# Kernel tuning notes

Hardware: AMD Instinct MI355X
Metric: run time of the kernel (lower is better)

The kernel has to match this reference:

```python
import jax, jax.numpy as jnp
import numpy as np

# Config (mirrors init_kwargs)
N_PARTS = 4
N_DATASETS = 4
N_VOLUMES = 12
N_TRANSFORMS = 1
TEMP = 0.1
EPS = 1e-6
BS = N_PARTS * N_DATASETS * N_VOLUMES          # 192
N = BS * (N_TRANSFORMS + 1)                    # 384 total rows
PD = N_PARTS * N_DATASETS                      # 16
C, H, W = 32, 48, 48


def setup_inputs() -> dict:
    key = jax.random.key(0)
    k1, k2 = jax.random.split(key)
    reg_pred = jax.random.normal(k1, (N, C, H, W), dtype=jnp.float32)
    mean_representations = jax.random.normal(k2, (N_DATASETS, C, H, W), dtype=jnp.float32)
    return {"reg_pred": reg_pred, "mean_representations": mean_representations}


def reference(reg_pred, mean_representations):
    X = reg_pred.reshape(N, -1)                                  # [N, D]
    ds_id = (jnp.arange(N) // N_PARTS) % N_DATASETS              # dataset id per row
    Mn = mean_representations.reshape(N_DATASETS, -1)[ds_id]     # [N, D] per-row mean
    Z = X - Mn                                                   # demeaned
    # cosine similarity with per-vector norm clamped at eps (torch CosineSimilarity)
    nrm = jnp.maximum(jnp.linalg.norm(Z, axis=1), EPS)
    Zn = Z / nrm[:, None]
    S = (Zn @ Zn.T) / TEMP                                       # [N, N] scaled cos sims
    E = jnp.exp(S)
    # negative (denominator) set for anchor a: all j with j % PD != a % PD
    rem = jnp.arange(N) % PD
    neg_mask = rem[:, None] != rem[None, :]
    Dsum = jnp.sum(E * neg_mask, axis=1)                         # [N]

    p = jnp.arange(BS)
    i1 = p
    i2 = BS + p
    i3 = (p + PD) % N
    i4 = (BS + p + PD) % N

    def pair_loss(a, b):
        # Faithful to original: BOTH terms use the (a,b) numerator similarity
        num = S[a, b]
        en = jnp.exp(num)
        return -(num - jnp.log(en + Dsum[a])) - (num - jnp.log(en + Dsum[b]))

    total = (pair_loss(i1, i2) + pair_loss(i3, i4)
             + pair_loss(i1, i3) + pair_loss(i2, i4)).sum()
    return total / (N_TRANSFORMS * 3 * BS)
```

## Files before the change

kernel.cpp:

```cpp
#include <hip/hip_runtime.h>
#include <hip/hip_bf16.h>
#include <stdint.h>

#define NR 384
#define DD 73728
#define PDV 16
#define KSPLIT 128
#define KCH 576
#define BK 32
#define NIT 18
#define RS 40
#define TILE_F 16384
#define KSTRIDE (9 * TILE_F)

typedef __bf16 bf16;
typedef __attribute__((ext_vector_type(4))) __bf16 bf16x4;
typedef __attribute__((ext_vector_type(8))) __bf16 bf16x8;
typedef __attribute__((ext_vector_type(4))) float f32x4;

__global__ __launch_bounds__(256, 3) void k_gram(const float* __restrict__ X,
                                                 const float* __restrict__ M,
                                                 float* __restrict__ Gp9,
                                                 float* __restrict__ Dp,
                                                 unsigned* __restrict__ ctr) {
    __shared__ float msh[4 * KCH];
    __shared__ __align__(16) char sbuf[41984];
    bf16* ash = (bf16*)sbuf;
    bf16* bsh = (bf16*)(sbuf + 20480);

    const int tid  = threadIdx.x;
    const int lane = tid & 63;
    const int w    = tid >> 6;
    const int quad = lane >> 4;
    const int l15  = lane & 15;
    const int wm   = w & 1, wn = w >> 1;
    const int srow = tid >> 3;
    const int fseg = tid & 7;
    const int mds  = (srow >> 2) & 3;

    if (blockIdx.x == 0 && tid == 0) *ctr = 0u;

    int xcd  = blockIdx.x & 7;
    int g    = blockIdx.x >> 3;
    int tile = g % 6;
    int ks   = xcd + 8 * (g / 6);
    int tm = (tile < 3) ? 0 : ((tile < 5) ? 1 : 2);
    int tn = (tile < 3) ? tile : ((tile < 5) ? (tile - 2) : 2);
    const bool diag = (tm == tn);
    const float* Xa = X + (size_t)(tm * 128) * DD;
    const float* Xb = X + (size_t)(tn * 128) * DD;
    size_t k0 = (size_t)ks * KCH;

    for (int i = tid; i < 4 * 144; i += 256) {
        int ds = i / 144;
        int c  = (i - ds * 144) * 4;
        *(float4*)&msh[ds * KCH + c] = *(const float4*)(M + (size_t)ds * DD + k0 + c);
    }

    f32x4 acc[4][4];
#pragma unroll
    for (int i = 0; i < 4; ++i)
#pragma unroll
        for (int j = 0; j < 4; ++j) acc[i][j] = (f32x4){0.f, 0.f, 0.f, 0.f};

    float4 xa[4], xb[4];
    auto load_regs = [&](int it) {
        size_t gk = k0 + (size_t)it * BK + fseg * 4;
#pragma unroll
        for (int p = 0; p < 4; ++p) {
            int row = p * 32 + srow;
            xa[p] = *(const float4*)(Xa + (size_t)row * DD + gk);
            if (!diag) xb[p] = *(const float4*)(Xb + (size_t)row * DD + gk);
        }
    };
    auto write_tiles = [&](int it, int buf) {
        int kc = it * BK + fseg * 4;
        float4 m4 = *(const float4*)&msh[mds * KCH + kc];
#pragma unroll
        for (int p = 0; p < 4; ++p) {
            int row = p * 32 + srow;
            bf16x4 za;
            za[0] = (bf16)(xa[p].x - m4.x); za[1] = (bf16)(xa[p].y - m4.y);
            za[2] = (bf16)(xa[p].z - m4.z); za[3] = (bf16)(xa[p].w - m4.w);
            *(bf16x4*)&ash[buf * 5120 + row * RS + fseg * 4] = za;
            if (!diag) {
                bf16x4 zb;
                zb[0] = (bf16)(xb[p].x - m4.x); zb[1] = (bf16)(xb[p].y - m4.y);
                zb[2] = (bf16)(xb[p].z - m4.z); zb[3] = (bf16)(xb[p].w - m4.w);
                *(bf16x4*)&bsh[buf * 5120 + row * RS + fseg * 4] = zb;
            }
        }
    };
    auto compute = [&](int buf) {
        const bf16* bb = diag ? (ash + buf * 5120) : (bsh + buf * 5120);
        bf16x8 af[4], bfv[4];
#pragma unroll
        for (int i = 0; i < 4; ++i) {
            int r = wm * 64 + i * 16 + l15;
            af[i] = *(const bf16x8*)&ash[buf * 5120 + r * RS + quad * 8];
        }
#pragma unroll
        for (int j = 0; j < 4; ++j) {
            int r = wn * 64 + j * 16 + l15;
            bfv[j] = *(const bf16x8*)&bb[r * RS + quad * 8];
        }
#pragma unroll
        for (int i = 0; i < 4; ++i)
#pragma unroll
            for (int j = 0; j < 4; ++j)
                acc[i][j] = __builtin_amdgcn_mfma_f32_16x16x32_bf16(
                    af[i], bfv[j], acc[i][j], 0, 0, 0);
    };

    load_regs(0);
    __syncthreads();
    write_tiles(0, 0);
    load_regs(1);
    __syncthreads();

    for (int it = 0; it < NIT; ++it) {
        int buf = it & 1;
        if (it + 1 < NIT) {
            write_tiles(it + 1, buf ^ 1);
            if (it + 2 < NIT) load_regs(it + 2);
        }
        compute(buf);
        __syncthreads();
    }

    float* gp = Gp9 + (size_t)ks * KSTRIDE + (size_t)(tm * 3 + tn) * TILE_F;
#pragma unroll
    for (int i = 0; i < 4; ++i) {
        int lr0 = wm * 64 + i * 16 + quad * 4;
#pragma unroll
        for (int j = 0; j < 4; ++j) {
            int lc = wn * 64 + j * 16 + l15;
#pragma unroll
            for (int r = 0; r < 4; ++r)
                gp[(lr0 + r) * 128 + lc] = acc[i][j][r];
        }
    }

    if (diag) {
        if (wm == wn && (l15 >> 2) == quad) {
#pragma unroll
            for (int i = 0; i < 4; ++i)
                Dp[(size_t)ks * NR + tm * 128 + wm * 64 + i * 16 + l15] =
                    acc[i][i][l15 & 3];
        }
    } else {
        float* tb = (float*)sbuf;
        float* gpT = Gp9 + (size_t)ks * KSTRIDE + (size_t)(tn * 3 + tm) * TILE_F;
#pragma unroll
        for (int h = 0; h < 2; ++h) {
            __syncthreads();
            if (wm == h) {
#pragma unroll
                for (int i = 0; i < 4; ++i) {
                    int rr0 = i * 16 + quad * 4;
#pragma unroll
                    for (int j = 0; j < 4; ++j) {
                        int cc = wn * 64 + j * 16 + l15;
#pragma unroll
                        for (int r = 0; r < 4; ++r)
                            tb[(rr0 + r) * 129 + cc] = acc[i][j][r];
                    }
                }
            }
            __syncthreads();
#pragma unroll
            for (int rep = 0; rep < 32; ++rep) {
                int idx = rep * 256 + tid;
                int c = idx >> 6;
                int r = idx & 63;
                gpT[c * 128 + h * 64 + r] = tb[r * 129 + c];
            }
        }
    }
}

__global__ __launch_bounds__(384) void k_tail(const float* __restrict__ Gp9,
                                              const float* __restrict__ Dp,
                                              float* __restrict__ rt,
                                              unsigned* __restrict__ ctr,
                                              float* __restrict__ out) {
    __shared__ float invn_sh[NR];
    __shared__ float sv[NR];
    __shared__ float wred[6];
    __shared__ bool amlast;

    const int tid  = threadIdx.x;
    const int lane = tid & 63;
    const int w    = tid >> 6;
    const int b    = tid;
    const int a    = blockIdx.x;

    float s2 = 0.f;
    const float* dp = Dp + b;
#pragma unroll 8
    for (int ks = 0; ks < KSPLIT; ++ks) s2 += dp[(size_t)ks * NR];
    invn_sh[b] = 1.f / fmaxf(sqrtf(s2), 1e-6f);
    __syncthreads();

    const int pa = a >> 7, pb = b >> 7;
    const float* gbase = Gp9 + (size_t)(pa * 3 + pb) * TILE_F
                       + (size_t)(a & 127) * 128 + (b & 127);
    float gsum = 0.f;
#pragma unroll 8
    for (int ks = 0; ks < KSPLIT; ++ks) gsum += gbase[(size_t)ks * KSTRIDE];

    const float ia = invn_sh[a];
    const float s  = gsum * ia * invn_sh[b] * 10.0f;
    sv[b] = s;
    float e = ((b & 15) != (a & 15)) ? expf(s) : 0.f;
#pragma unroll
    for (int o = 32; o > 0; o >>= 1) e += __shfl_down(e, o);
    if (lane == 0) wred[w] = e;
    __syncthreads();

    if (tid == 0) {
        float Dsa = wred[0] + wred[1] + wred[2] + wred[3] + wred[4] + wred[5];
        int pr[4];
        if (a < 16)       { pr[0] = 192 + a; pr[1] = a + 16;  pr[2] = a + 192; pr[3] = a + 368; }
        else if (a < 192) { pr[0] = 192 + a; pr[1] = a + 16;  pr[2] = a + 192; pr[3] = a - 16; }
        else if (a < 368) { pr[0] = a - 192; pr[1] = a + 16;  pr[2] = a - 192; pr[3] = a - 16; }
        else              { pr[0] = a - 192; pr[1] = a - 368; pr[2] = a - 192; pr[3] = a - 16; }
        float t = 0.f;
#pragma unroll
        for (int sidx = 0; sidx < 4; ++sidx) {
            float num = sv[pr[sidx]];
            t += -num + logf(expf(num) + Dsa);
        }
        rt[a] = t;
        __threadfence();
        amlast = (atomicAdd(ctr, 1u) == (unsigned)(NR - 1));
    }
    __syncthreads();

    if (amlast) {
        __threadfence();
        float v = rt[tid];
#pragma unroll
        for (int o = 32; o > 0; o >>= 1) v += __shfl_down(v, o);
        if (lane == 0) wred[w] = v;
        __syncthreads();
        if (tid == 0)
            out[0] = (wred[0] + wred[1] + wred[2] + wred[3] + wred[4] + wred[5])
                     * (1.0f / 576.0f);
    }
}

extern "C" void kernel_launch(void* const* d_in, const int* in_sizes, int n_in,
                              void* d_out, int out_size, void* d_ws, size_t ws_size,
                              hipStream_t stream) {
    const float* X = (const float*)d_in[0];
    const float* M = (const float*)d_in[1];
    float* out = (float*)d_out;

    char* ws = (char*)d_ws;
    float* Gp9 = (float*)ws;
    float* Dp  = Gp9 + (size_t)KSPLIT * KSTRIDE;
    float* rt  = Dp + (size_t)KSPLIT * NR;
    unsigned* ctr = (unsigned*)(rt + NR);

    k_gram<<<dim3(6 * KSPLIT), dim3(256), 0, stream>>>(X, M, Gp9, Dp, ctr);
    k_tail<<<dim3(NR), dim3(384), 0, stream>>>(Gp9, Dp, rt, ctr, out);
}
```

Measured before the change: 205.1 us.

## Fuse gram and tail kernels with a grid-wide atomic barrier

```diff
diff --git a/kernel.cpp b/kernel.cpp
--- a/kernel.cpp
+++ b/kernel.cpp
@@ -4,7 +4,6 @@
 
 #define NR 384
 #define DD 73728
-#define PDV 16
 #define KSPLIT 128
 #define KCH 576
 #define BK 32
@@ -12,18 +11,26 @@
 #define RS 40
 #define TILE_F 16384
 #define KSTRIDE (9 * TILE_F)
+#define NBLK (6 * KSPLIT)
 
 typedef __bf16 bf16;
 typedef __attribute__((ext_vector_type(4))) __bf16 bf16x4;
 typedef __attribute__((ext_vector_type(8))) __bf16 bf16x8;
 typedef __attribute__((ext_vector_type(4))) float f32x4;
 
-__global__ __launch_bounds__(256, 3) void k_gram(const float* __restrict__ X,
-                                                 const float* __restrict__ M,
-                                                 float* __restrict__ Gp9,
-                                                 float* __restrict__ Dp,
-                                                 unsigned* __restrict__ ctr) {
-    __shared__ float msh[4 * KCH];
+__device__ __forceinline__ void bar_lgkm() {
+    asm volatile("s_waitcnt lgkmcnt(0)" ::: "memory");
+    __builtin_amdgcn_s_barrier();
+    asm volatile("" ::: "memory");
+}
+
+__global__ __launch_bounds__(256, 3) void k_all(const float* __restrict__ X,
+                                                const float* __restrict__ M,
+                                                float* __restrict__ Gp9,
+                                                float* __restrict__ Dp,
+                                                float* __restrict__ rt,
+                                                unsigned* __restrict__ ctr,
+                                                float* __restrict__ out) {
     __shared__ __align__(16) char sbuf[41984];
     bf16* ash = (bf16*)sbuf;
     bf16* bsh = (bf16*)(sbuf + 20480);
@@ -38,8 +45,6 @@
     const int fseg = tid & 7;
     const int mds  = (srow >> 2) & 3;
 
-    if (blockIdx.x == 0 && tid == 0) *ctr = 0u;
-
     int xcd  = blockIdx.x & 7;
     int g    = blockIdx.x >> 3;
     int tile = g % 6;
@@ -49,23 +54,19 @@
     const bool diag = (tm == tn);
     const float* Xa = X + (size_t)(tm * 128) * DD;
     const float* Xb = X + (size_t)(tn * 128) * DD;
+    const float* Mr = M + (size_t)mds * DD;
     size_t k0 = (size_t)ks * KCH;
 
-    for (int i = tid; i < 4 * 144; i += 256) {
-        int ds = i / 144;
-        int c  = (i - ds * 144) * 4;
-        *(float4*)&msh[ds * KCH + c] = *(const float4*)(M + (size_t)ds * DD + k0 + c);
-    }
-
     f32x4 acc[4][4];
 #pragma unroll
     for (int i = 0; i < 4; ++i)
 #pragma unroll
         for (int j = 0; j < 4; ++j) acc[i][j] = (f32x4){0.f, 0.f, 0.f, 0.f};
 
-    float4 xa[4], xb[4];
+    float4 xa[4], xb[4], m4;
     auto load_regs = [&](int it) {
         size_t gk = k0 + (size_t)it * BK + fseg * 4;
+        m4 = *(const float4*)(Mr + gk);
 #pragma unroll
         for (int p = 0; p < 4; ++p) {
             int row = p * 32 + srow;
@@ -74,8 +75,6 @@
         }
     };
     auto write_tiles = [&](int it, int buf) {
-        int kc = it * BK + fseg * 4;
-        float4 m4 = *(const float4*)&msh[mds * KCH + kc];
 #pragma unroll
         for (int p = 0; p < 4; ++p) {
             int row = p * 32 + srow;
@@ -113,10 +112,9 @@
     };
 
     load_regs(0);
-    __syncthreads();
     write_tiles(0, 0);
     load_regs(1);
-    __syncthreads();
+    bar_lgkm();
 
     for (int it = 0; it < NIT; ++it) {
         int buf = it & 1;
@@ -125,7 +123,7 @@
             if (it + 2 < NIT) load_regs(it + 2);
         }
         compute(buf);
-        __syncthreads();
+        bar_lgkm();
     }
 
     float* gp = Gp9 + (size_t)ks * KSTRIDE + (size_t)(tm * 3 + tn) * TILE_F;
@@ -153,7 +151,7 @@
         float* gpT = Gp9 + (size_t)ks * KSTRIDE + (size_t)(tn * 3 + tm) * TILE_F;
 #pragma unroll
         for (int h = 0; h < 2; ++h) {
-            __syncthreads();
+            bar_lgkm();
             if (wm == h) {
 #pragma unroll
                 for (int i = 0; i < 4; ++i) {
@@ -167,7 +165,7 @@
                     }
                 }
             }
-            __syncthreads();
+            bar_lgkm();
 #pragma unroll
             for (int rep = 0; rep < 32; ++rep) {
                 int idx = rep * 256 + tid;
@@ -177,49 +175,60 @@
             }
         }
     }
-}
-
-__global__ __launch_bounds__(384) void k_tail(const float* __restrict__ Gp9,
-                                              const float* __restrict__ Dp,
-                                              float* __restrict__ rt,
-                                              unsigned* __restrict__ ctr,
-                                              float* __restrict__ out) {
-    __shared__ float invn_sh[NR];
-    __shared__ float sv[NR];
-    __shared__ float wred[6];
-    __shared__ bool amlast;
-
-    const int tid  = threadIdx.x;
-    const int lane = tid & 63;
-    const int w    = tid >> 6;
-    const int b    = tid;
-    const int a    = blockIdx.x;
-
-    float s2 = 0.f;
-    const float* dp = Dp + b;
+
+    __syncthreads();
+    if (tid == 0) {
+        __threadfence();
+        __hip_atomic_fetch_add(ctr, 1u, __ATOMIC_RELEASE,
+                               __HIP_MEMORY_SCOPE_AGENT);
+    }
+    if (blockIdx.x >= NR) return;
+
+    if (tid == 0) {
+        while (__hip_atomic_load(ctr, __ATOMIC_ACQUIRE,
+                                 __HIP_MEMORY_SCOPE_AGENT) < (unsigned)NBLK)
+            __builtin_amdgcn_s_sleep(2);
+        __threadfence();
+    }
+    __syncthreads();
+
+    float* invn_sh = (float*)sbuf;
+    float* sv      = (float*)(sbuf + 1536);
+    float* wred    = (float*)(sbuf + 3072);
+    int*   lastf   = (int*)(sbuf + 3088);
+
+    const int a  = blockIdx.x;
+    const int pa = a >> 7;
+
+    for (int b = tid; b < NR; b += 256) {
+        float s2 = 0.f;
+        const float* dp = Dp + b;
 #pragma unroll 8
-    for (int ks = 0; ks < KSPLIT; ++ks) s2 += dp[(size_t)ks * NR];
-    invn_sh[b] = 1.f / fmaxf(sqrtf(s2), 1e-6f);
-    __syncthreads();
-
-    const int pa = a >> 7, pb = b >> 7;
-    const float* gbase = Gp9 + (size_t)(pa * 3 + pb) * TILE_F
-                       + (size_t)(a & 127) * 128 + (b & 127);
-    float gsum = 0.f;
+        for (int kk = 0; kk < KSPLIT; ++kk) s2 += dp[(size_t)kk * NR];
+        invn_sh[b] = 1.f / fmaxf(sqrtf(s2), 1e-6f);
+    }
+    __syncthreads();
+
+    const float ia = invn_sh[a];
+    float eacc = 0.f;
+    for (int b = tid; b < NR; b += 256) {
+        const int pb = b >> 7;
+        const float* gbase = Gp9 + (size_t)(pa * 3 + pb) * TILE_F
+                           + (size_t)(a & 127) * 128 + (b & 127);
+        float gsum = 0.f;
 #pragma unroll 8
-    for (int ks = 0; ks < KSPLIT; ++ks) gsum += gbase[(size_t)ks * KSTRIDE];
-
-    const float ia = invn_sh[a];
-    const float s  = gsum * ia * invn_sh[b] * 10.0f;
-    sv[b] = s;
-    float e = ((b & 15) != (a & 15)) ? expf(s) : 0.f;
-#pragma unroll
-    for (int o = 32; o > 0; o >>= 1) e += __shfl_down(e, o);
-    if (lane == 0) wred[w] = e;
+        for (int kk = 0; kk < KSPLIT; ++kk) gsum += gbase[(size_t)kk * KSTRIDE];
+        float s = gsum * ia * invn_sh[b] * 10.0f;
+        sv[b] = s;
+        if ((b & 15) != (a & 15)) eacc += expf(s);
+    }
+#pragma unroll
+    for (int o = 32; o > 0; o >>= 1) eacc += __shfl_down(eacc, o);
+    if (lane == 0) wred[w] = eacc;
     __syncthreads();
 
     if (tid == 0) {
-        float Dsa = wred[0] + wred[1] + wred[2] + wred[3] + wred[4] + wred[5];
+        float Dsa = wred[0] + wred[1] + wred[2] + wred[3];
         int pr[4];
         if (a < 16)       { pr[0] = 192 + a; pr[1] = a + 16;  pr[2] = a + 192; pr[3] = a + 368; }
         else if (a < 192) { pr[0] = 192 + a; pr[1] = a + 16;  pr[2] = a + 192; pr[3] = a - 16; }
@@ -233,20 +242,21 @@
         }
         rt[a] = t;
         __threadfence();
-        amlast = (atomicAdd(ctr, 1u) == (unsigned)(NR - 1));
-    }
-    __syncthreads();
-
-    if (amlast) {
-        __threadfence();
-        float v = rt[tid];
+        unsigned prev = __hip_atomic_fetch_add(ctr + 1, 1u, __ATOMIC_ACQ_REL,
+                                               __HIP_MEMORY_SCOPE_AGENT);
+        *lastf = (prev == (unsigned)(NR - 1));
+    }
+    __syncthreads();
+
+    if (*lastf) {
+        __threadfence();
+        float v = rt[tid] + ((tid < NR - 256) ? rt[256 + tid] : 0.0f);
 #pragma unroll
         for (int o = 32; o > 0; o >>= 1) v += __shfl_down(v, o);
         if (lane == 0) wred[w] = v;
         __syncthreads();
         if (tid == 0)
-            out[0] = (wred[0] + wred[1] + wred[2] + wred[3] + wred[4] + wred[5])
-                     * (1.0f / 576.0f);
+            out[0] = (wred[0] + wred[1] + wred[2] + wred[3]) * (1.0f / 576.0f);
     }
 }
 
@@ -263,6 +273,6 @@
     float* rt  = Dp + (size_t)KSPLIT * NR;
     unsigned* ctr = (unsigned*)(rt + NR);
 
-    k_gram<<<dim3(6 * KSPLIT), dim3(256), 0, stream>>>(X, M, Gp9, Dp, ctr);
-    k_tail<<<dim3(NR), dim3(384), 0, stream>>>(Gp9, Dp, rt, ctr, out);
+    hipMemsetAsync(ctr, 0, 2 * sizeof(unsigned), stream);
+    k_all<<<dim3(NBLK), dim3(256), 0, stream>>>(X, M, Gp9, Dp, rt, ctr, out);
 }
```

Result: slower. 375.6 us (+83.1%).
